# Performance work log

Measured on AMD Instinct MI355X. Metric: run time of the kernel, lower is better.

## Reference

```python
import jax, jax.numpy as jnp
import numpy as np

H = 512      # hidden_size == embedding_dim (required by the module's MHA)
V = 8000     # vocab_size
NH = 8       # num_heads
HD = H // NH # head_dim


def setup_inputs() -> dict:
    key = jax.random.key(0)
    ks = jax.random.split(key, 16)
    B, S, SRC = 64, 128, 256
    sc = 0.02
    return {
        "encoded_features": jax.random.normal(ks[0], (B, SRC, H), jnp.float32),
        "prev_chars": jax.random.randint(ks[1], (B, S), 0, V),
        "hidden0": jnp.zeros((B, H), jnp.float32),
        # learned params
        "embedding": jax.random.normal(ks[2], (V, H), jnp.float32) * sc,
        "in_proj_w": jax.random.normal(ks[3], (3 * H, H), jnp.float32) * sc,  # MHA packed q,k,v
        "in_proj_b": jnp.zeros((3 * H,), jnp.float32),
        "out_proj_w": jax.random.normal(ks[4], (H, H), jnp.float32) * sc,
        "out_proj_b": jnp.zeros((H,), jnp.float32),
        "gru_w_ih": jax.random.normal(ks[5], (3 * H, H + H), jnp.float32) * sc,  # input = [emb; attn]
        "gru_w_hh": jax.random.normal(ks[6], (3 * H, H), jnp.float32) * sc,
        "gru_b_ih": jnp.zeros((3 * H,), jnp.float32),
        "gru_b_hh": jnp.zeros((3 * H,), jnp.float32),
        "proj_w": jax.random.normal(ks[7], (V, H), jnp.float32) * sc,
        "proj_b": jnp.zeros((V,), jnp.float32),
    }


def _mha(q_in, kv, in_proj_w, in_proj_b, out_proj_w, out_proj_b):
    # torch nn.MultiheadAttention, batch_first=True, self q / cross kv
    wq, wk, wv = jnp.split(in_proj_w, 3, axis=0)
    bq, bk, bv = jnp.split(in_proj_b, 3, axis=0)
    B, S, _ = q_in.shape
    L = kv.shape[1]
    q = (q_in @ wq.T + bq).reshape(B, S, NH, HD)
    k = (kv @ wk.T + bk).reshape(B, L, NH, HD)
    v = (kv @ wv.T + bv).reshape(B, L, NH, HD)
    scores = jnp.einsum("bshd,blhd->bhsl", q, k) / np.sqrt(HD).astype(np.float32)
    attn = jax.nn.softmax(scores, axis=-1)
    ctx = jnp.einsum("bhsl,blhd->bshd", attn, v).reshape(B, S, H)
    return ctx @ out_proj_w.T + out_proj_b


def _gru_scan(gru_input, h0, w_ih, w_hh, b_ih, b_hh):
    # gru_input: [B, S, 2H]; torch GRUCell math, scanned over time
    def step(h, x_t):
        gi = x_t @ w_ih.T + b_ih
        gh = h @ w_hh.T + b_hh
        i_r, i_z, i_n = jnp.split(gi, 3, axis=-1)
        h_r, h_z, h_n = jnp.split(gh, 3, axis=-1)
        r = jax.nn.sigmoid(i_r + h_r)
        z = jax.nn.sigmoid(i_z + h_z)
        n = jnp.tanh(i_n + r * h_n)
        h_new = (1.0 - z) * n + z * h
        return h_new, h_new

    _, hs = jax.lax.scan(step, h0, jnp.swapaxes(gru_input, 0, 1))  # [S,B,H]
    return jnp.swapaxes(hs, 0, 1)  # [B,S,H]


def reference(encoded_features, prev_chars, hidden0, embedding, in_proj_w, in_proj_b,
              out_proj_w, out_proj_b, gru_w_ih, gru_w_hh, gru_b_ih, gru_b_hh, proj_w, proj_b):
    B, S = prev_chars.shape
    char_emb = embedding[prev_chars]                      # [B,S,H]
    query_input = char_emb + hidden0[:, None, :]          # dims match (H == E)
    attn_out = _mha(query_input, encoded_features, in_proj_w, in_proj_b, out_proj_w, out_proj_b)
    gru_input = jnp.concatenate([char_emb, attn_out], axis=-1)  # [B,S,2H]
    hidden_states = _gru_scan(gru_input, hidden0, gru_w_ih, gru_w_hh, gru_b_ih, gru_b_hh)
    logits = hidden_states @ proj_w.T + proj_b            # dropout is identity in eval
    probs = jax.nn.softmax(logits, axis=-1)
    return probs, hidden_states
```

## Files before the change

kernel.cpp:

```cpp
#include <hip/hip_runtime.h>
#include <hip/hip_bf16.h>
#include <hip/hip_cooperative_groups.h>

namespace cg = cooperative_groups;

#define BB 64
#define SS 128
#define LSRC 256
#define HH 512
#define NHEAD 8
#define HDIM 64
#define VV 8000
#define M1 (BB*SS)
#define M2 (BB*LSRC)

typedef unsigned short u16;
typedef __attribute__((ext_vector_type(8))) short bf16x8;
typedef __attribute__((ext_vector_type(4))) float f32x4;

__device__ __forceinline__ float b2f(u16 u){
    unsigned int x = ((unsigned int)u) << 16;
    return __uint_as_float(x);
}
__device__ __forceinline__ u16 f2b(float f){
    unsigned int x = __float_as_uint(f);
    x = x + 0x7fffu + ((x >> 16) & 1u);
    return (u16)(x >> 16);
}

__global__ __launch_bounds__(256) void k_probe(const u16* __restrict__ emb, int* __restrict__ flag){
    __shared__ int tot;
    if (threadIdx.x == 0) tot = 0;
    __syncthreads();
    int cnt = 0;
    #pragma unroll
    for (int i = 0; i < 32; i++){
        u16 u = emb[threadIdx.x * 32 + i];
        cnt += (((u >> 7) & 0xFF) >= 0x80);
    }
    #pragma unroll
    for (int off = 1; off < 64; off <<= 1) cnt += __shfl_xor(cnt, off);
    if ((threadIdx.x & 63) == 0) atomicAdd(&tot, cnt);
    __syncthreads();
    if (threadIdx.x == 0) *flag = (tot > 100) ? 1 : 0;
}

__global__ __launch_bounds__(256) void k_convert(const void* __restrict__ src, u16* __restrict__ dst,
                                                 const int* __restrict__ flag, long n8){
    long i = (long)blockIdx.x * 256 + threadIdx.x;
    if (i >= n8) return;
    if (*flag){
        const float4* s = (const float4*)src;
        float4 a = s[i*2], b = s[i*2+1];
        u16 o[8] = { f2b(a.x), f2b(a.y), f2b(a.z), f2b(a.w), f2b(b.x), f2b(b.y), f2b(b.z), f2b(b.w) };
        *(uint4*)(dst + i*8) = *(const uint4*)o;
    } else {
        *(uint4*)(dst + i*8) = ((const uint4*)src)[i];
    }
}

__global__ __launch_bounds__(256) void k_embed(const int* __restrict__ pc,
    const u16* __restrict__ emb, const u16* __restrict__ h0,
    u16* __restrict__ gruin, u16* __restrict__ qin)
{
    int c = blockIdx.x * 256 + threadIdx.x;
    int row = c >> 6;
    int kc = (c & 63) << 3;
    int b = row >> 7;
    int tok = pc[row];
    uint4 e = *(const uint4*)(emb + (long)tok * HH + kc);
    *(uint4*)(gruin + (long)row * (2*HH) + kc) = e;
    uint4 hv = *(const uint4*)(h0 + b * HH + kc);
    const u16* ep = (const u16*)&e;
    const u16* hp = (const u16*)&hv;
    u16 q[8];
    #pragma unroll
    for (int j = 0; j < 8; j++) q[j] = f2b(b2f(ep[j]) + b2f(hp[j]));
    *(uint4*)(qin + (long)row * HH + kc) = *(const uint4*)q;
}

__global__ __launch_bounds__(256) void gemm_bt(
    const u16* __restrict__ A, int lda,
    const u16* __restrict__ W, int ldw,
    const u16* __restrict__ bias,
    u16* __restrict__ Cb, float* __restrict__ Cf, int ldc,
    int N, int K)
{
    __shared__ u16 As[128*64];
    __shared__ u16 Bs[128*64];
    const int tid = threadIdx.x;
    const int wave = tid >> 6, lane = tid & 63;
    const int m0 = blockIdx.x * 128, n0 = blockIdx.y * 128;
    const int wm = (wave & 1) * 64, wn = (wave >> 1) * 64;
    const int lm = lane & 15, lq = lane >> 4;
    f32x4 acc[4][4];
    #pragma unroll
    for (int i = 0; i < 4; i++)
        #pragma unroll
        for (int j = 0; j < 4; j++) acc[i][j] = (f32x4){0.f,0.f,0.f,0.f};

    for (int k0 = 0; k0 < K; k0 += 64) {
        #pragma unroll
        for (int i = 0; i < 4; i++) {
            int chunk = i*256 + tid;
            int row = chunk >> 3, kc = (chunk & 7) << 3;
            *(uint4*)(As + chunk*8) = *(const uint4*)(A + (long)(m0+row)*lda + k0 + kc);
            int brow = n0 + row; if (brow >= N) brow = N - 1;
            *(uint4*)(Bs + chunk*8) = *(const uint4*)(W + (long)brow*ldw + k0 + kc);
        }
        __syncthreads();
        #pragma unroll
        for (int kk = 0; kk < 64; kk += 32) {
            bf16x8 af[4], bfr[4];
            #pragma unroll
            for (int i = 0; i < 4; i++){
                af[i]  = *(const bf16x8*)(As + (wm + i*16 + lm)*64 + kk + lq*8);
                bfr[i] = *(const bf16x8*)(Bs + (wn + i*16 + lm)*64 + kk + lq*8);
            }
            #pragma unroll
            for (int mi = 0; mi < 4; mi++)
                #pragma unroll
                for (int ni = 0; ni < 4; ni++)
                    acc[mi][ni] = __builtin_amdgcn_mfma_f32_16x16x32_bf16(af[mi], bfr[ni], acc[mi][ni], 0, 0, 0);
        }
        __syncthreads();
    }
    #pragma unroll
    for (int ni = 0; ni < 4; ni++){
        int n = n0 + wn + ni*16 + lm;
        if (n >= N) continue;
        float bv = bias ? b2f(bias[n]) : 0.f;
        #pragma unroll
        for (int mi = 0; mi < 4; mi++){
            #pragma unroll
            for (int r = 0; r < 4; r++){
                int m = m0 + wm + mi*16 + lq*4 + r;
                float v = acc[mi][ni][r] + bv;
                if (Cf) Cf[(long)m*ldc + n] = v;
                else    Cb[(long)m*ldc + n] = f2b(v);
            }
        }
    }
}

__global__ __launch_bounds__(256) void k_attn(const u16* __restrict__ Qb,
    const u16* __restrict__ Kb, const u16* __restrict__ Vb, u16* __restrict__ ctxb)
{
    __shared__ u16 smem[64*264 + 4*32*264];
    u16* Vt = smem;
    u16* Ks = smem + 64*264;
    u16* Ps = smem + 64*264;
    const int bid = blockIdx.x;
    const int h = bid & 7, b = bid >> 3;
    const int tid = threadIdx.x;
    const int wave = tid >> 6, lane = tid & 63;
    const int lm = lane & 15, lq = lane >> 4;
    const long kvbase = (long)b*LSRC*HH + h*HDIM;

    #pragma unroll
    for (int i = 0; i < 8; i++){
        int c = i*256 + tid;
        int l = c >> 3, ch0 = (c & 7) << 3;
        uint4 kv = *(const uint4*)(Kb + kvbase + (long)l*HH + ch0);
        *(uint4*)(Ks + l*72 + ch0) = kv;
        uint4 vv = *(const uint4*)(Vb + kvbase + (long)l*HH + ch0);
        const u16* vp = (const u16*)&vv;
        #pragma unroll
        for (int j = 0; j < 8; j++) Vt[(ch0 + j)*264 + l] = vp[j];
    }

    bf16x8 aq[2][2];
    #pragma unroll
    for (int mt = 0; mt < 2; mt++)
        #pragma unroll
        for (int kk = 0; kk < 2; kk++)
            aq[mt][kk] = *(const bf16x8*)(Qb + (long)(b*SS + wave*32 + mt*16 + lm)*HH
                                              + h*HDIM + kk*32 + lq*8);
    __syncthreads();

    f32x4 accs[2][16];
    #pragma unroll
    for (int mt = 0; mt < 2; mt++)
        #pragma unroll
        for (int nt = 0; nt < 16; nt++) accs[mt][nt] = (f32x4){0.f,0.f,0.f,0.f};
    #pragma unroll
    for (int nt = 0; nt < 16; nt++){
        bf16x8 bk0 = *(const bf16x8*)(Ks + (nt*16 + lm)*72 +  0 + lq*8);
        bf16x8 bk1 = *(const bf16x8*)(Ks + (nt*16 + lm)*72 + 32 + lq*8);
        #pragma unroll
        for (int mt = 0; mt < 2; mt++){
            accs[mt][nt] = __builtin_amdgcn_mfma_f32_16x16x32_bf16(aq[mt][0], bk0, accs[mt][nt], 0, 0, 0);
            accs[mt][nt] = __builtin_amdgcn_mfma_f32_16x16x32_bf16(aq[mt][1], bk1, accs[mt][nt], 0, 0, 0);
        }
    }

    float mxv[2][4];
    #pragma unroll
    for (int mt = 0; mt < 2; mt++)
        #pragma unroll
        for (int r = 0; r < 4; r++){
            float m = -1e30f;
            #pragma unroll
            for (int nt = 0; nt < 16; nt++) m = fmaxf(m, accs[mt][nt][r]);
            m *= 0.125f;
            m = fmaxf(m, __shfl_xor(m, 1));
            m = fmaxf(m, __shfl_xor(m, 2));
            m = fmaxf(m, __shfl_xor(m, 4));
            m = fmaxf(m, __shfl_xor(m, 8));
            mxv[mt][r] = m;
        }
    float smv[2][4] = {{0.f,0.f,0.f,0.f},{0.f,0.f,0.f,0.f}};
    #pragma unroll
    for (int mt = 0; mt < 2; mt++)
        #pragma unroll
        for (int nt = 0; nt < 16; nt++)
            #pragma unroll
            for (int r = 0; r < 4; r++){
                float p = __expf(accs[mt][nt][r]*0.125f - mxv[mt][r]);
                smv[mt][r] += p;
                accs[mt][nt][r] = p;
            }
    float inv[2][4];
    #pragma unroll
    for (int mt = 0; mt < 2; mt++)
        #pragma unroll
        for (int r = 0; r < 4; r++){
            float s = smv[mt][r];
            s += __shfl_xor(s, 1); s += __shfl_xor(s, 2);
            s += __shfl_xor(s, 4); s += __shfl_xor(s, 8);
            inv[mt][r] = 1.f / s;
        }

    __syncthreads();
    const int woff = wave * (32*264);
    #pragma unroll
    for (int mt = 0; mt < 2; mt++)
        #pragma unroll
        for (int nt = 0; nt < 16; nt++)
            #pragma unroll
            for (int r = 0; r < 4; r++)
                Ps[woff + (mt*16 + lq*4 + r)*264 + nt*16 + lm] = f2b(accs[mt][nt][r]);
    __syncthreads();

    f32x4 accc[2][4];
    #pragma unroll
    for (int mt = 0; mt < 2; mt++)
        #pragma unroll
        for (int nt = 0; nt < 4; nt++) accc[mt][nt] = (f32x4){0.f,0.f,0.f,0.f};
    #pragma unroll
    for (int kk = 0; kk < 8; kk++){
        bf16x8 pa0 = *(const bf16x8*)(Ps + woff + ( 0 + lm)*264 + kk*32 + lq*8);
        bf16x8 pa1 = *(const bf16x8*)(Ps + woff + (16 + lm)*264 + kk*32 + lq*8);
        #pragma unroll
        for (int nt = 0; nt < 4; nt++){
            bf16x8 bv = *(const bf16x8*)(Vt + (nt*16 + lm)*264 + kk*32 + lq*8);
            accc[0][nt] = __builtin_amdgcn_mfma_f32_16x16x32_bf16(pa0, bv, accc[0][nt], 0, 0, 0);
            accc[1][nt] = __builtin_amdgcn_mfma_f32_16x16x32_bf16(pa1, bv, accc[1][nt], 0, 0, 0);
        }
    }

    #pragma unroll
    for (int mt = 0; mt < 2; mt++)
        #pragma unroll
        for (int nt = 0; nt < 4; nt++)
            #pragma unroll
            for (int r = 0; r < 4; r++){
                int srow = wave*32 + mt*16 + lq*4 + r;
                int ch = nt*16 + lm;
                float v = accc[mt][nt][r] * inv[mt][r];
                ctxb[(long)(b*SS + srow)*HH + h*HDIM + ch] = f2b(v);
            }
}

__global__ __launch_bounds__(256) void k_gru_all(
    const float* __restrict__ gi, const u16* __restrict__ whh, const u16* __restrict__ bhh,
    const u16* __restrict__ h0b, u16* __restrict__ hx0, u16* __restrict__ hx1,
    u16* __restrict__ hout)
{
    cg::grid_group grid = cg::this_grid();
    __shared__ u16 wlds[48*520];
    __shared__ u16 hlds[64*520];
    const int tid = threadIdx.x;
    const int j0 = blockIdx.x * 16;
    const int wave = tid >> 6, lane = tid & 63;
    const int lm = lane & 15, lq = lane >> 4;

    #pragma unroll
    for (int i = 0; i < 12; i++){
        int c = i*256 + tid;
        int rl = c >> 6, kc = (c & 63) << 3;
        int g = rl >> 4, jr = rl & 15;
        *(uint4*)(wlds + rl*520 + kc) = *(const uint4*)(whh + (long)(g*512 + j0 + jr)*HH + kc);
    }

    const int j = j0 + lm;
    const float br = b2f(bhh[j]), bz = b2f(bhh[512 + j]), bn = b2f(bhh[1024 + j]);
    float hp[4];
    #pragma unroll
    for (int r = 0; r < 4; r++){
        int b = wave*16 + lq*4 + r;
        hp[r] = b2f(h0b[b*HH + j]);
    }
    const int brow = wave*16 + lm;

    const u16* hsrc = h0b;
    for (int s = 0; s < SS; s++){
        float gir[4], giz[4], gin[4];
        #pragma unroll
        for (int r = 0; r < 4; r++){
            int b = wave*16 + lq*4 + r;
            long gbase = (long)(b*SS + s)*1536;
            gir[r] = gi[gbase + j];
            giz[r] = gi[gbase + 512 + j];
            gin[r] = gi[gbase + 1024 + j];
        }
        #pragma unroll
        for (int i = 0; i < 16; i++){
            int c = i*256 + tid;
            int row = c >> 6, kc = (c & 63) << 3;
            *(uint4*)(hlds + row*520 + kc) = *(const uint4*)(hsrc + row*HH + kc);
        }
        __syncthreads();
        f32x4 acc[3];
        acc[0] = (f32x4){0.f,0.f,0.f,0.f};
        acc[1] = acc[0]; acc[2] = acc[0];
        #pragma unroll
        for (int k0 = 0; k0 < 512; k0 += 32){
            bf16x8 a = *(const bf16x8*)(hlds + brow*520 + k0 + lq*8);
            #pragma unroll
            for (int g = 0; g < 3; g++){
                bf16x8 wf = *(const bf16x8*)(wlds + (g*16 + lm)*520 + k0 + lq*8);
                acc[g] = __builtin_amdgcn_mfma_f32_16x16x32_bf16(a, wf, acc[g], 0, 0, 0);
            }
        }
        u16* hdst = (s & 1) ? hx1 : hx0;
        #pragma unroll
        for (int r = 0; r < 4; r++){
            int b = wave*16 + lq*4 + r;
            float rg = 1.f/(1.f + __expf(-(gir[r] + acc[0][r] + br)));
            float zg = 1.f/(1.f + __expf(-(giz[r] + acc[1][r] + bz)));
            float ng = tanhf(gin[r] + rg*(acc[2][r] + bn));
            float hv = (1.f - zg)*ng + zg*hp[r];
            hp[r] = hv;
            u16 hb = f2b(hv);
            hdst[b*HH + j] = hb;
            hout[(long)(b*SS + s)*HH + j] = hb;
        }
        hsrc = hdst;
        grid.sync();
    }
}

__global__ __launch_bounds__(256) void k_softmax(const u16* __restrict__ logits, void* __restrict__ out,
                                                 const int* __restrict__ flag)
{
    __shared__ float red[4];
    __shared__ float red2[4];
    long row = blockIdx.x;
    const u16* p = logits + row*VV;
    int tid = threadIdx.x, wave = tid >> 6, lane = tid & 63;
    float v[32];
    float mx = -1e30f;
    #pragma unroll
    for (int i = 0; i < 32; i++){
        int c = tid + i*256;
        v[i] = (c < VV) ? b2f(p[c]) : -1e30f;
        mx = fmaxf(mx, v[i]);
    }
    #pragma unroll
    for (int off = 1; off < 64; off <<= 1) mx = fmaxf(mx, __shfl_xor(mx, off));
    if (lane == 0) red[wave] = mx;
    __syncthreads();
    mx = fmaxf(fmaxf(red[0], red[1]), fmaxf(red[2], red[3]));
    float sum = 0.f;
    #pragma unroll
    for (int i = 0; i < 32; i++){
        int c = tid + i*256;
        if (c < VV){ v[i] = __expf(v[i] - mx); sum += v[i]; }
    }
    #pragma unroll
    for (int off = 1; off < 64; off <<= 1) sum += __shfl_xor(sum, off);
    if (lane == 0) red2[wave] = sum;
    __syncthreads();
    float inv = 1.f / (red2[0] + red2[1] + red2[2] + red2[3]);
    int f = *flag;
    float* pf = (float*)out + row*VV;
    u16*  pb = (u16*)out + row*VV;
    #pragma unroll
    for (int i = 0; i < 32; i++){
        int c = tid + i*256;
        if (c < VV){
            float r = v[i]*inv;
            if (f) pf[c] = r; else pb[c] = f2b(r);
        }
    }
}

__global__ __launch_bounds__(256) void k_hidout(const u16* __restrict__ hid, void* __restrict__ out,
                                                const int* __restrict__ flag)
{
    long i = (long)blockIdx.x * 256 + threadIdx.x;
    u16 h = hid[i];
    if (*flag) ((float*)out + (size_t)M1*VV)[i] = b2f(h);
    else       ((u16*)out  + (size_t)M1*VV)[i] = h;
}

extern "C" void kernel_launch(void* const* d_in, const int* in_sizes, int n_in,
                              void* d_out, int out_size, void* d_ws, size_t ws_size,
                              hipStream_t stream)
{
    const int* pc = (const int*)d_in[1];

    const size_t MB = 1u << 20;
    char* w = (char*)d_ws;
    u16* qin   = (u16*)(w + 0);
    u16* ctxb  = (u16*)(w + 0);
    u16* Qb    = (u16*)(w + 8*MB);
    u16* Kb    = (u16*)(w + 16*MB);
    u16* Vb    = (u16*)(w + 32*MB);
    u16* gruin = (u16*)(w + 48*MB);
    float* gi  = (float*)(w + 0);
    u16* logits= (u16*)(w + 0);
    u16* enc_b = (u16*)(w + 126*MB);
    u16* emb_b = (u16*)(w + 142*MB);
    u16* pw_b  = (u16*)(w + 150*MB);
    u16* wih_b = (u16*)(w + 158*MB);
    u16* whh_b = (u16*)(w + 161*MB);
    u16* ipw_b = (u16*)(w + 163*MB);
    u16* opw_b = (u16*)(w + 165*MB);
    u16* h0_b  = (u16*)(w + 166*MB);
    u16* ipb_b = (u16*)(w + 166*MB + 128*1024);
    u16* opb_b = (u16*)(w + 166*MB + 192*1024);
    u16* bih_b = (u16*)(w + 166*MB + 256*1024);
    u16* bhh_b = (u16*)(w + 166*MB + 320*1024);
    u16* pb_b  = (u16*)(w + 166*MB + 384*1024);
    int* flag  = (int*)(w + 166*MB + 448*1024);
    u16* hx0   = (u16*)(w + 167*MB);
    u16* hx1   = (u16*)(w + 167*MB + 128*1024);
    u16* hid_b = (u16*)(w + 168*MB);

    k_probe<<<1, 256, 0, stream>>>((const u16*)d_in[3], flag);
    struct { const void* s; u16* d; long n; } cv[13] = {
        { d_in[0],  enc_b, (long)M2*HH },
        { d_in[2],  h0_b,  BB*HH },
        { d_in[3],  emb_b, (long)VV*HH },
        { d_in[4],  ipw_b, 3*HH*HH },
        { d_in[5],  ipb_b, 3*HH },
        { d_in[6],  opw_b, HH*HH },
        { d_in[7],  opb_b, HH },
        { d_in[8],  wih_b, 3L*HH*2*HH },
        { d_in[9],  whh_b, 3*HH*HH },
        { d_in[10], bih_b, 3*HH },
        { d_in[11], bhh_b, 3*HH },
        { d_in[12], pw_b,  (long)VV*HH },
        { d_in[13], pb_b,  VV },
    };
    for (int i = 0; i < 13; i++){
        long n8 = cv[i].n >> 3;
        k_convert<<<(int)((n8 + 255)/256), 256, 0, stream>>>(cv[i].s, cv[i].d, flag, n8);
    }

    k_embed<<<2048, 256, 0, stream>>>(pc, emb_b, h0_b, gruin, qin);
    gemm_bt<<<dim3(64,4),  256, 0, stream>>>(qin,   HH, ipw_b,            HH, ipb_b,      Qb,  nullptr, HH,  HH, HH);
    gemm_bt<<<dim3(128,4), 256, 0, stream>>>(enc_b, HH, ipw_b + 512*512,  HH, ipb_b+512,  Kb,  nullptr, HH,  HH, HH);
    gemm_bt<<<dim3(128,4), 256, 0, stream>>>(enc_b, HH, ipw_b + 1024*512, HH, ipb_b+1024, Vb,  nullptr, HH,  HH, HH);
    k_attn<<<BB*NHEAD, 256, 0, stream>>>(Qb, Kb, Vb, ctxb);
    gemm_bt<<<dim3(64,4),  256, 0, stream>>>(ctxb, HH, opw_b, HH, opb_b, gruin + 512, nullptr, 2*HH, HH, HH);
    gemm_bt<<<dim3(64,12), 256, 0, stream>>>(gruin, 2*HH, wih_b, 2*HH, bih_b, nullptr, gi, 1536, 1536, 2*HH);

    {
        const float* gia = gi; const u16* whha = whh_b; const u16* bhha = bhh_b;
        const u16* h0a = h0_b; u16* hx0a = hx0; u16* hx1a = hx1; u16* hida = hid_b;
        void* gru_args[] = { (void*)&gia, (void*)&whha, (void*)&bhha, (void*)&h0a,
                             (void*)&hx0a, (void*)&hx1a, (void*)&hida };
        hipLaunchCooperativeKernel((const void*)k_gru_all, dim3(32), dim3(256),
                                   gru_args, 0, stream);
    }

    gemm_bt<<<dim3(64,63), 256, 0, stream>>>(hid_b, HH, pw_b, HH, pb_b, logits, nullptr, VV, VV, HH);
    k_softmax<<<M1, 256, 0, stream>>>(logits, d_out, flag);
    k_hidout<<<16384, 256, 0, stream>>>(hid_b, d_out, flag);
}
```

Baseline: 1.765 ms.

## Replace grid.sync with custom atomic barrier and load hidden state directly into registers

```diff
diff --git a/kernel.cpp b/kernel.cpp
--- a/kernel.cpp
+++ b/kernel.cpp
@@ -1,8 +1,5 @@
 #include <hip/hip_runtime.h>
 #include <hip/hip_bf16.h>
-#include <hip/hip_cooperative_groups.h>
-
-namespace cg = cooperative_groups;
 
 #define BB 64
 #define SS 128
@@ -28,9 +25,11 @@
     return (u16)(x >> 16);
 }
 
-__global__ __launch_bounds__(256) void k_probe(const u16* __restrict__ emb, int* __restrict__ flag){
+__global__ __launch_bounds__(256) void k_probe(const u16* __restrict__ emb, int* __restrict__ flag,
+                                               int* __restrict__ bar){
     __shared__ int tot;
     if (threadIdx.x == 0) tot = 0;
+    if (threadIdx.x < 16) bar[threadIdx.x] = 0;
     __syncthreads();
     int cnt = 0;
     #pragma unroll
@@ -275,11 +274,9 @@
 __global__ __launch_bounds__(256) void k_gru_all(
     const float* __restrict__ gi, const u16* __restrict__ whh, const u16* __restrict__ bhh,
     const u16* __restrict__ h0b, u16* __restrict__ hx0, u16* __restrict__ hx1,
-    u16* __restrict__ hout)
-{
-    cg::grid_group grid = cg::this_grid();
+    u16* __restrict__ hout, int* __restrict__ bar)
+{
     __shared__ u16 wlds[48*520];
-    __shared__ u16 hlds[64*520];
     const int tid = threadIdx.x;
     const int j0 = blockIdx.x * 16;
     const int wave = tid >> 6, lane = tid & 63;
@@ -292,19 +289,21 @@
         int g = rl >> 4, jr = rl & 15;
         *(uint4*)(wlds + rl*520 + kc) = *(const uint4*)(whh + (long)(g*512 + j0 + jr)*HH + kc);
     }
+    __syncthreads();
 
     const int j = j0 + lm;
     const float br = b2f(bhh[j]), bz = b2f(bhh[512 + j]), bn = b2f(bhh[1024 + j]);
+    const int brow = wave*16 + lm;
     float hp[4];
     #pragma unroll
-    for (int r = 0; r < 4; r++){
-        int b = wave*16 + lq*4 + r;
-        hp[r] = b2f(h0b[b*HH + j]);
-    }
-    const int brow = wave*16 + lm;
+    for (int r = 0; r < 4; r++) hp[r] = b2f(h0b[(wave*16 + lq*4 + r)*HH + j]);
 
     const u16* hsrc = h0b;
     for (int s = 0; s < SS; s++){
+        bf16x8 af[16];
+        #pragma unroll
+        for (int k = 0; k < 16; k++)
+            af[k] = *(const bf16x8*)(hsrc + (long)brow*HH + k*32 + lq*8);
         float gir[4], giz[4], gin[4];
         #pragma unroll
         for (int r = 0; r < 4; r++){
@@ -314,23 +313,15 @@
             giz[r] = gi[gbase + 512 + j];
             gin[r] = gi[gbase + 1024 + j];
         }
-        #pragma unroll
-        for (int i = 0; i < 16; i++){
-            int c = i*256 + tid;
-            int row = c >> 6, kc = (c & 63) << 3;
-            *(uint4*)(hlds + row*520 + kc) = *(const uint4*)(hsrc + row*HH + kc);
-        }
-        __syncthreads();
         f32x4 acc[3];
         acc[0] = (f32x4){0.f,0.f,0.f,0.f};
         acc[1] = acc[0]; acc[2] = acc[0];
         #pragma unroll
-        for (int k0 = 0; k0 < 512; k0 += 32){
-            bf16x8 a = *(const bf16x8*)(hlds + brow*520 + k0 + lq*8);
+        for (int k = 0; k < 16; k++){
             #pragma unroll
             for (int g = 0; g < 3; g++){
-                bf16x8 wf = *(const bf16x8*)(wlds + (g*16 + lm)*520 + k0 + lq*8);
-                acc[g] = __builtin_amdgcn_mfma_f32_16x16x32_bf16(a, wf, acc[g], 0, 0, 0);
+                bf16x8 wf = *(const bf16x8*)(wlds + (g*16 + lm)*520 + k*32 + lq*8);
+                acc[g] = __builtin_amdgcn_mfma_f32_16x16x32_bf16(af[k], wf, acc[g], 0, 0, 0);
             }
         }
         u16* hdst = (s & 1) ? hx1 : hx0;
@@ -346,8 +337,15 @@
             hdst[b*HH + j] = hb;
             hout[(long)(b*SS + s)*HH + j] = hb;
         }
+        __threadfence();
+        if (lane == 0){
+            atomicAdd(bar, 1);
+            const int target = 128*(s+1);
+            while (__hip_atomic_load(bar, __ATOMIC_RELAXED, __HIP_MEMORY_SCOPE_AGENT) < target)
+                __builtin_amdgcn_s_sleep(1);
+        }
+        __threadfence();
         hsrc = hdst;
-        grid.sync();
     }
 }
 
@@ -435,11 +433,12 @@
     u16* bhh_b = (u16*)(w + 166*MB + 320*1024);
     u16* pb_b  = (u16*)(w + 166*MB + 384*1024);
     int* flag  = (int*)(w + 166*MB + 448*1024);
+    int* bar   = (int*)(w + 166*MB + 452*1024);
     u16* hx0   = (u16*)(w + 167*MB);
     u16* hx1   = (u16*)(w + 167*MB + 128*1024);
     u16* hid_b = (u16*)(w + 168*MB);
 
-    k_probe<<<1, 256, 0, stream>>>((const u16*)d_in[3], flag);
+    k_probe<<<1, 256, 0, stream>>>((const u16*)d_in[3], flag, bar);
     struct { const void* s; u16* d; long n; } cv[13] = {
         { d_in[0],  enc_b, (long)M2*HH },
         { d_in[2],  h0_b,  BB*HH },
@@ -471,8 +470,9 @@
     {
         const float* gia = gi; const u16* whha = whh_b; const u16* bhha = bhh_b;
         const u16* h0a = h0_b; u16* hx0a = hx0; u16* hx1a = hx1; u16* hida = hid_b;
+        int* bara = bar;
         void* gru_args[] = { (void*)&gia, (void*)&whha, (void*)&bhha, (void*)&h0a,
-                             (void*)&hx0a, (void*)&hx1a, (void*)&hida };
+                             (void*)&hx0a, (void*)&hx1a, (void*)&hida, (void*)&bara };
         hipLaunchCooperativeKernel((const void*)k_gru_all, dim3(32), dim3(256),
                                    gru_args, 0, stream);
     }
```

After: 2.356 ms. +33.5%, slower.
